# Optimization experiments

Hardware: AMD Instinct MI355X
Metric: run time of the kernel (lower is better)

## Reference

```python
import jax, jax.numpy as jnp
import numpy as np

N, E = 10000, 160000
IN, C, H = 64, 256, 8


def gat_layer(x, src, dst, W, a_src, a_dst, b, heads, ch, n, concat=True):
    # linear transform per head: [n, heads, ch]
    h = (x @ W).reshape(n, heads, ch)
    al_s = jnp.sum(h * a_src, axis=-1)  # [n, heads]
    al_d = jnp.sum(h * a_dst, axis=-1)  # [n, heads]
    e = jax.nn.leaky_relu(al_s[src] + al_d[dst], 0.2)  # [E, heads]
    # segment softmax over incoming edges of each dst node
    m = jax.ops.segment_max(e, dst, num_segments=n)
    m = jnp.where(jnp.isfinite(m), m, 0.0)  # guard empty segments
    p = jnp.exp(e - m[dst])
    s = jax.ops.segment_sum(p, dst, num_segments=n)
    alpha = p / (s[dst] + 1e-16)  # [E, heads]
    # scatter-aggregate weighted source features
    out = jax.ops.segment_sum(h[src] * alpha[:, :, None], dst, num_segments=n)
    out = out.reshape(n, heads * ch) if concat else out.mean(axis=1)
    return jax.nn.elu(out + b)


def setup_inputs() -> dict:
    key = jax.random.key(0)
    ks = jax.random.split(key, 16)
    sc = 0.05
    x = jax.random.normal(ks[0], (N, IN), dtype=jnp.float32)
    edge_index = jax.random.randint(ks[1], (2, E), 0, N)
    W1 = jax.random.normal(ks[2], (IN, H * C), dtype=jnp.float32) * sc
    as1 = jax.random.normal(ks[3], (H, C), dtype=jnp.float32) * sc
    ad1 = jax.random.normal(ks[4], (H, C), dtype=jnp.float32) * sc
    b1 = jnp.zeros((H * C,), dtype=jnp.float32)
    W2 = jax.random.normal(ks[5], (H * C, H * C), dtype=jnp.float32) * sc
    as2 = jax.random.normal(ks[6], (H, C), dtype=jnp.float32) * sc
    ad2 = jax.random.normal(ks[7], (H, C), dtype=jnp.float32) * sc
    b2 = jnp.zeros((H * C,), dtype=jnp.float32)
    W3 = jax.random.normal(ks[8], (H * C, C), dtype=jnp.float32) * sc
    as3 = jax.random.normal(ks[9], (1, C), dtype=jnp.float32) * sc
    ad3 = jax.random.normal(ks[10], (1, C), dtype=jnp.float32) * sc
    b3 = jnp.zeros((C,), dtype=jnp.float32)
    return {"x": x, "edge_index": edge_index,
            "W1": W1, "as1": as1, "ad1": ad1, "b1": b1,
            "W2": W2, "as2": as2, "ad2": ad2, "b2": b2,
            "W3": W3, "as3": as3, "ad3": ad3, "b3": b3}


def reference(x, edge_index, W1, as1, ad1, b1, W2, as2, ad2, b2, W3, as3, ad3, b3):
    src, dst = edge_index[0], edge_index[1]
    h = gat_layer(x, src, dst, W1, as1, ad1, b1, H, C, N, concat=True)
    h = gat_layer(h, src, dst, W2, as2, ad2, b2, H, C, N, concat=True)
    h = gat_layer(h, src, dst, W3, as3, ad3, b3, 1, C, N, concat=True)
    return h
```

## Files before the change

### kernel.cpp

```cpp
#include <hip/hip_runtime.h>


typedef __attribute__((ext_vector_type(8))) short bf16x8;
typedef __attribute__((ext_vector_type(4))) float f32x4;

#define DEVINL __device__ __forceinline__

static constexpr int NN   = 10000;
static constexpr int NE   = 160000;
static constexpr int MPAD = 10240;
static constexpr int DIN  = 64;
static constexpr int CCH  = 256;
static constexpr int NH   = 8;
static constexpr int F12  = 2048;

DEVINL unsigned short f2bf(float x){
  unsigned u = __float_as_uint(x);
  u += 0x7fffu + ((u >> 16) & 1u);
  return (unsigned short)(u >> 16);
}
DEVINL float bf2f(unsigned short h){ return __uint_as_float(((unsigned)h) << 16); }

DEVINL void gload_lds16(const unsigned short* g, unsigned short* lds){
  __builtin_amdgcn_global_load_lds(
      (__attribute__((address_space(1))) unsigned int*)(g),
      (__attribute__((address_space(3))) unsigned int*)(lds), 16, 0, 0);
}

__global__ __launch_bounds__(256) void transpose_cvt_kernel(const float* __restrict__ W,
                                                            unsigned short* __restrict__ Wt,
                                                            int K, int Nn){
  __shared__ float tile[32][33];
  int k0 = blockIdx.x*32, n0 = blockIdx.y*32;
  int tx = threadIdx.x & 31, ty = threadIdx.x >> 5;
  #pragma unroll
  for (int r = ty; r < 32; r += 8) tile[r][tx] = W[(size_t)(k0+r)*Nn + n0 + tx];
  __syncthreads();
  #pragma unroll
  for (int r = ty; r < 32; r += 8) Wt[(size_t)(n0+r)*K + k0 + tx] = f2bf(tile[tx][r]);
}

__global__ __launch_bounds__(256) void hist_kernel(const int* __restrict__ dst,
                                                   int* __restrict__ deg, int E_){
  int i = blockIdx.x*256 + threadIdx.x;
  if (i < E_) atomicAdd(&deg[dst[i]], 1);
}

__global__ __launch_bounds__(256) void scan_kernel(const int* __restrict__ deg,
                                                   int* __restrict__ off, int n){
  const int CH = (n + 255) / 256;
  int t = threadIdx.x;
  int lo = t*CH, hi = min(lo + CH, n);
  int s = 0;
  for (int i = lo; i < hi; i++) s += deg[i];
  __shared__ int ws[256];
  ws[t] = s;
  __syncthreads();
  for (int d = 1; d < 256; d <<= 1){
    int v = (t >= d) ? ws[t-d] : 0;
    __syncthreads();
    ws[t] += v;
    __syncthreads();
  }
  int run = ws[t] - s;
  for (int i = lo; i < hi; i++){ off[i] = run; run += deg[i]; }
  if (t == 255) off[n] = ws[255];
}

__global__ __launch_bounds__(256) void scatter_kernel(const int* __restrict__ src,
                                                      const int* __restrict__ dst,
                                                      const int* __restrict__ off,
                                                      int* __restrict__ cursor,
                                                      int* __restrict__ csrc, int E_){
  int i = blockIdx.x*256 + threadIdx.x;
  if (i >= E_) return;
  int d = dst[i];
  int pI = atomicAdd(&cursor[d], 1);
  csrc[off[d] + pI] = src[i];
}

__global__ __launch_bounds__(256) void wa1_kernel(const float* __restrict__ W1,
                                                  const float* __restrict__ a1s,
                                                  const float* __restrict__ a1d,
                                                  float* __restrict__ Wa1){
  int t = blockIdx.x*256 + threadIdx.x;
  if (t >= 64*16) return;
  int c = t >> 4, i = t & 15;
  int h = i & 7;
  const float* a = (i < 8) ? a1s : a1d;
  float s = 0.f;
  #pragma unroll 8
  for (int j = 0; j < 256; j++) s = fmaf(W1[(size_t)c*F12 + h*256 + j], a[h*256 + j], s);
  Wa1[c*16 + i] = s;
}

__global__ __launch_bounds__(256) void logits1_kernel(const float* __restrict__ x,
                                                      const float* __restrict__ Wa1,
                                                      float* __restrict__ als,
                                                      float* __restrict__ ald){
  __shared__ float wa[64*16];
  for (int i = threadIdx.x; i < 64*16; i += 256) wa[i] = Wa1[i];
  __syncthreads();
  int gid = blockIdx.x*256 + threadIdx.x;
  int v = gid >> 4, i = gid & 15;
  if (v >= NN) return;
  float s = 0.f;
  #pragma unroll
  for (int c = 0; c < 64; c++) s = fmaf(x[(size_t)v*64 + c], wa[c*16 + i], s);
  if (i < 8) als[v*8 + i] = s;
  else       ald[v*8 + (i - 8)] = s;
}

__global__ __launch_bounds__(256) void agg1_kernel(const float* __restrict__ x,
                                                   const int* __restrict__ off,
                                                   const int* __restrict__ csrc,
                                                   const float* __restrict__ als,
                                                   const float* __restrict__ ald,
                                                   unsigned short* __restrict__ Xa){
  const int wv = threadIdx.x >> 6, lane = threadIdx.x & 63;
  const int v = blockIdx.x*4 + wv;
  if (v >= NN) return;
  const int e0 = off[v], deg = off[v+1] - e0;

  float aldv[8];
  #pragma unroll
  for (int h = 0; h < 8; h++) aldv[h] = ald[v*8 + h];

  float m[8], s[8];
  #pragma unroll
  for (int h = 0; h < 8; h++){ m[h] = -1e30f; s[h] = 0.f; }
  for (int base = 0; base < deg; base += 64){
    int i = base + lane;
    bool act = i < deg;
    int u = act ? csrc[e0 + i] : 0;
    float e[8];
    #pragma unroll
    for (int h = 0; h < 8; h++){
      float xe = act ? (als[u*8 + h] + aldv[h]) : -1e30f;
      e[h] = xe > 0.f ? xe : 0.2f*xe;
    }
    #pragma unroll
    for (int h = 0; h < 8; h++){
      float t = e[h];
      #pragma unroll
      for (int d = 1; d < 64; d <<= 1) t = fmaxf(t, __shfl_xor(t, d));
      float nm = fmaxf(m[h], t);
      float cs = act ? __expf(e[h] - nm) : 0.f;
      #pragma unroll
      for (int d = 1; d < 64; d <<= 1) cs += __shfl_xor(cs, d);
      s[h] = s[h]*__expf(m[h] - nm) + cs;
      m[h] = nm;
    }
  }
  float sinv[8];
  #pragma unroll
  for (int h = 0; h < 8; h++) sinv[h] = 1.f / (s[h] + 1e-16f);

  float acc[8];
  #pragma unroll
  for (int h = 0; h < 8; h++) acc[h] = 0.f;
  for (int j = 0; j < deg; j++){
    int u = csrc[e0 + j];
    float xv = x[(size_t)u*64 + lane];
    #pragma unroll
    for (int h = 0; h < 8; h++){
      float xe = als[u*8 + h] + aldv[h];
      xe = xe > 0.f ? xe : 0.2f*xe;
      float a = __expf(xe - m[h]) * sinv[h];
      acc[h] = fmaf(a, xv, acc[h]);
    }
  }
  #pragma unroll
  for (int h = 0; h < 8; h++)
    Xa[(size_t)v*512 + h*64 + lane] = f2bf(acc[h]);
}

__global__ __launch_bounds__(256) void gemm_l1_kernel(
    const unsigned short* __restrict__ Xa,
    const unsigned short* __restrict__ Wt1,
    const float* __restrict__ b1,
    unsigned short* __restrict__ actA)
{
  __shared__ __align__(16) unsigned short As[2][128*32];
  __shared__ __align__(16) unsigned short Bs[2][256*32];
  const int wave = threadIdx.x >> 6, lane = threadIdx.x & 63;
  const int wm = wave >> 1, wn = wave & 1;
  const size_t m0 = (size_t)blockIdx.x * 128;
  const int h = blockIdx.y;
  const int lr = lane >> 2, l3 = lane & 3;

  #pragma unroll
  for (int sB = 0; sB < 2; sB++){
    #pragma unroll
    for (int j = 0; j < 2; j++){
      int rb = (wave*2 + j)*16;
      int row = rb + lr;
      int kc = l3 ^ ((row >> 1) & 3);
      gload_lds16(Xa + (m0 + row)*512 + h*64 + sB*32 + kc*8, &As[sB][rb*32]);
    }
    #pragma unroll
    for (int j = 0; j < 4; j++){
      int rb = (wave*4 + j)*16;
      int row = rb + lr;
      int kc = l3 ^ ((row >> 1) & 3);
      gload_lds16(Wt1 + (size_t)(h*256 + row)*64 + sB*32 + kc*8, &Bs[sB][rb*32]);
    }
  }
  asm volatile("s_waitcnt vmcnt(0)" ::: "memory");
  __syncthreads();

  f32x4 acc[4][8];
  #pragma unroll
  for (int i = 0; i < 4; i++)
    #pragma unroll
    for (int j = 0; j < 8; j++) acc[i][j] = (f32x4){0.f,0.f,0.f,0.f};

  const int rl = lane & 15, q = lane >> 4;
  #pragma unroll
  for (int sB = 0; sB < 2; sB++){
    bf16x8 af[4], bfr[8];
    #pragma unroll
    for (int mm = 0; mm < 4; mm++){
      int row = wm*64 + mm*16 + rl;
      int ch = q ^ ((row >> 1) & 3);
      af[mm] = *(const bf16x8*)&As[sB][row*32 + ch*8];
    }
    #pragma unroll
    for (int n = 0; n < 8; n++){
      int row = wn*128 + n*16 + rl;
      int ch = q ^ ((row >> 1) & 3);
      bfr[n] = *(const bf16x8*)&Bs[sB][row*32 + ch*8];
    }
    #pragma unroll
    for (int mm = 0; mm < 4; mm++)
      #pragma unroll
      for (int n = 0; n < 8; n++)
        acc[mm][n] = __builtin_amdgcn_mfma_f32_16x16x32_bf16(af[mm], bfr[n], acc[mm][n], 0, 0, 0);
  }

  #pragma unroll
  for (int mm = 0; mm < 4; mm++)
    #pragma unroll
    for (int n = 0; n < 8; n++)
      #pragma unroll
      for (int r = 0; r < 4; r++){
        size_t row = m0 + wm*64 + mm*16 + q*4 + r;
        int col = wn*128 + n*16 + rl;
        float o = acc[mm][n][r] + b1[h*256 + col];
        o = o > 0.f ? o : (__expf(o) - 1.f);
        actA[row*F12 + h*256 + col] = f2bf(o);
      }
}

__global__ __launch_bounds__(512, 1) void gemm_l2_kernel(
    const unsigned short* __restrict__ A,
    const unsigned short* __restrict__ Bt,
    unsigned short* __restrict__ Chm,
    int K)
{
  __shared__ __align__(16) unsigned short As[3][640*32];
  __shared__ __align__(16) unsigned short Bs[3][128*32];

  const int tid  = threadIdx.x;
  const int wave = tid >> 6, lane = tid & 63;
  const int wm = wave >> 1, wn = wave & 1;

  const int orig = blockIdx.x;
  const int wg   = (orig & 7) * 32 + (orig >> 3);
  const size_t m0 = (size_t)(wg >> 4) * 640;
  const size_t n0 = (size_t)(wg & 15) * 128;

  f32x4 acc[10][4];
  #pragma unroll
  for (int i = 0; i < 10; i++)
    #pragma unroll
    for (int j = 0; j < 4; j++) acc[i][j] = (f32x4){0.f,0.f,0.f,0.f};

  const int lr = lane >> 2;
  const int l3 = lane & 3;

  auto stageA = [&](int slot, int k0, int j){
    const int rb  = (wave*5 + j) * 16;
    const int row = rb + lr;
    const int kc  = l3 ^ ((row >> 1) & 3);
    gload_lds16(A + (m0 + row)*(size_t)K + k0 + kc*8, &As[slot][rb*32]);
  };
  auto stageB = [&](int slot, int k0){
    const int rb  = wave * 16;
    const int row = rb + lr;
    const int kc  = l3 ^ ((row >> 1) & 3);
    gload_lds16(Bt + (n0 + row)*(size_t)K + k0 + kc*8, &Bs[slot][rb*32]);
  };
  auto stageTile = [&](int T){
    const int slot = T % 3, k0 = T << 5;
    #pragma unroll
    for (int j = 0; j < 5; j++) stageA(slot, k0, j);
    stageB(slot, k0);
  };

  const int nt = K >> 5;
  stageTile(0);
  stageTile(1);

  const int rl = lane & 15;
  const int q  = lane >> 4;

  for (int T = 0; T < nt; ++T){
    if (T + 1 < nt) asm volatile("s_waitcnt vmcnt(6)" ::: "memory");
    else            asm volatile("s_waitcnt vmcnt(0)" ::: "memory");
    __builtin_amdgcn_s_barrier();

    const int slot = T % 3;
    const bool st  = (T + 2 < nt);
    const int s2   = (T + 2) % 3;
    const int k2   = (T + 2) << 5;

    bf16x8 bfr[4], af[5];
    #pragma unroll
    for (int n = 0; n < 4; n++){
      const int row = wn*64 + n*16 + rl;
      const int ch  = q ^ ((row >> 1) & 3);
      bfr[n] = *(const bf16x8*)&Bs[slot][row*32 + ch*8];
    }
    #pragma unroll
    for (int m = 0; m < 5; m++){
      const int row = wm*160 + m*16 + rl;
      const int ch  = q ^ ((row >> 1) & 3);
      af[m] = *(const bf16x8*)&As[slot][row*32 + ch*8];
    }
    if (st){ stageA(s2, k2, 0); stageA(s2, k2, 1); stageA(s2, k2, 2); }
    asm volatile("s_waitcnt lgkmcnt(0)" ::: "memory");
    __builtin_amdgcn_sched_barrier(0);
    __builtin_amdgcn_s_setprio(1);
    #pragma unroll
    for (int m = 0; m < 5; m++)
      #pragma unroll
      for (int n = 0; n < 4; n++)
        acc[m][n] = __builtin_amdgcn_mfma_f32_16x16x32_bf16(af[m], bfr[n], acc[m][n], 0, 0, 0);
    __builtin_amdgcn_s_setprio(0);
    __builtin_amdgcn_sched_barrier(0);
    #pragma unroll
    for (int m = 0; m < 5; m++){
      const int row = wm*160 + (m+5)*16 + rl;
      const int ch  = q ^ ((row >> 1) & 3);
      af[m] = *(const bf16x8*)&As[slot][row*32 + ch*8];
    }
    if (st){ stageA(s2, k2, 3); stageA(s2, k2, 4); stageB(s2, k2); }
    asm volatile("s_waitcnt lgkmcnt(0)" ::: "memory");
    __builtin_amdgcn_sched_barrier(0);
    __builtin_amdgcn_s_setprio(1);
    #pragma unroll
    for (int m = 0; m < 5; m++)
      #pragma unroll
      for (int n = 0; n < 4; n++)
        acc[m+5][n] = __builtin_amdgcn_mfma_f32_16x16x32_bf16(af[m], bfr[n], acc[m+5][n], 0, 0, 0);
    __builtin_amdgcn_s_setprio(0);
  }

  const int head = (int)(n0 >> 8);
  #pragma unroll
  for (int m = 0; m < 10; m++)
    #pragma unroll
    for (int n = 0; n < 4; n++)
      #pragma unroll
      for (int r = 0; r < 4; r++){
        size_t row = m0 + wm*160 + m*16 + q*4 + r;
        size_t col = n0 + wn*64  + n*16 + rl;
        int ch = (int)(col & 255);
        Chm[((size_t)head*MPAD + row)*CCH + ch] = f2bf(acc[m][n][r]);
      }
}

__global__ __launch_bounds__(256, 2) void gemm_bt_kernel(
    const unsigned short* __restrict__ A,
    const unsigned short* __restrict__ Bt,
    unsigned short* __restrict__ C,
    int K, int Nn)
{
  __shared__ __align__(16) unsigned short As[2][128*32];
  __shared__ __align__(16) unsigned short Bs[2][128*32];
  const int tid  = threadIdx.x;
  const int wave = tid >> 6, lane = tid & 63;
  const int wr = wave >> 1, wc = wave & 1;
  const size_t m0 = (size_t)blockIdx.x * 128;
  const size_t n0 = (size_t)blockIdx.y * 128;

  const int l4 = lane >> 2;
  const int lc = lane & 3;

  f32x4 acc[4][4];
  #pragma unroll
  for (int i = 0; i < 4; i++)
    #pragma unroll
    for (int j = 0; j < 4; j++) acc[i][j] = (f32x4){0.f,0.f,0.f,0.f};

  auto stage = [&](int buf, int kt){
    const int k0 = kt << 5;
    #pragma unroll
    for (int half = 0; half < 2; ++half){
      const int rb  = (wave + half*4) * 16;
      const int row = rb + l4;
      const int kc  = lc ^ ((row >> 1) & 3);
      gload_lds16(A + ((m0 + row)*(size_t)K + k0 + kc*8), &As[buf][rb*32]);
    }
    #pragma unroll
    for (int half = 0; half < 2; ++half){
      const int rb  = (wave + half*4) * 16;
      const int row = rb + l4;
      const int kc  = lc ^ ((row >> 1) & 3);
      gload_lds16(Bt + ((n0 + row)*(size_t)K + k0 + kc*8), &Bs[buf][rb*32]);
    }
  };

  const int nt = K >> 5;
  stage(0, 0);
  __syncthreads();

  const int rl = lane & 15;
  const int q  = lane >> 4;

  int cur = 0;
  for (int t = 0; t < nt; ++t){
    if (t + 1 < nt) stage(cur ^ 1, t + 1);
    bf16x8 af[4], bfr[4];
    #pragma unroll
    for (int m = 0; m < 4; m++){
      int row = wr*64 + m*16 + rl;
      int ch  = q ^ ((row >> 1) & 3);
      af[m] = *(const bf16x8*)&As[cur][row*32 + ch*8];
    }
    #pragma unroll
    for (int n = 0; n < 4; n++){
      int row = wc*64 + n*16 + rl;
      int ch  = q ^ ((row >> 1) & 3);
      bfr[n] = *(const bf16x8*)&Bs[cur][row*32 + ch*8];
    }
    #pragma unroll
    for (int m = 0; m < 4; m++)
      #pragma unroll
      for (int n = 0; n < 4; n++)
        acc[m][n] = __builtin_amdgcn_mfma_f32_16x16x32_bf16(af[m], bfr[n], acc[m][n], 0, 0, 0);
    __syncthreads();
    cur ^= 1;
  }

  #pragma unroll
  for (int m = 0; m < 4; m++)
    #pragma unroll
    for (int n = 0; n < 4; n++)
      #pragma unroll
      for (int r = 0; r < 4; r++){
        size_t row = m0 + wr*64 + m*16 + q*4 + r;
        size_t col = n0 + wc*64 + n*16 + rl;
        C[row*(size_t)Nn + col] = f2bf(acc[m][n][r]);
      }
}

__global__ __launch_bounds__(256) void logits_kernel(const unsigned short* __restrict__ Hm,
                                                     const float* __restrict__ aws,
                                                     const float* __restrict__ awd,
                                                     float* __restrict__ als,
                                                     float* __restrict__ ald,
                                                     int heads){
  int gw   = (blockIdx.x*256 + threadIdx.x) >> 6;
  int lane = threadIdx.x & 63;
  int node = gw / heads;
  int head = gw - node*heads;
  if (node >= NN) return;
  const unsigned short* hp = Hm + ((size_t)head*MPAD + node)*CCH + lane*4;
  const float* wsp = aws + head*CCH + lane*4;
  const float* wdp = awd + head*CCH + lane*4;
  float s = 0.f, d = 0.f;
  #pragma unroll
  for (int j = 0; j < 4; j++){
    float hv = bf2f(hp[j]);
    s = fmaf(hv, wsp[j], s);
    d = fmaf(hv, wdp[j], d);
  }
  #pragma unroll
  for (int m = 1; m < 64; m <<= 1){ s += __shfl_xor(s, m); d += __shfl_xor(d, m); }
  if (lane == 0){ als[node*heads + head] = s; ald[node*heads + head] = d; }
}

template<int NHD>
__global__ __launch_bounds__(256) void aggw_kernel(
    const unsigned short* __restrict__ Hm,
    const int* __restrict__ off, const int* __restrict__ csrc,
    const float* __restrict__ als, const float* __restrict__ ald,
    const float* __restrict__ bias,
    unsigned short* __restrict__ actout,
    float* __restrict__ fout)
{
  const int wv = threadIdx.x >> 6, lane = threadIdx.x & 63;
  int v, h;
  if constexpr (NHD == 8){
    h = blockIdx.x & 7;
    v = (blockIdx.x >> 3) * 4 + wv;
  } else {
    h = 0;
    v = blockIdx.x * 4 + wv;
  }
  if (v >= NN) return;
  const int e0 = off[v], deg = off[v+1] - e0;
  const float aldv = ald[v*NHD + h];

  __shared__ float al_sh[4][64];
  __shared__ int   u_sh[4][64];

  float mloc = -1e30f;
  for (int i = lane; i < deg; i += 64){
    int u = csrc[e0 + i];
    float xe = als[u*NHD + h] + aldv;
    xe = xe > 0.f ? xe : 0.2f*xe;
    mloc = fmaxf(mloc, xe);
  }
  #pragma unroll
  for (int d = 1; d < 64; d <<= 1) mloc = fmaxf(mloc, __shfl_xor(mloc, d));
  float sloc = 0.f;
  for (int i = lane; i < deg; i += 64){
    int u = csrc[e0 + i];
    float xe = als[u*NHD + h] + aldv;
    xe = xe > 0.f ? xe : 0.2f*xe;
    sloc += __expf(xe - mloc);
  }
  #pragma unroll
  for (int d = 1; d < 64; d <<= 1) sloc += __shfl_xor(sloc, d);
  const float sinv = 1.f / (sloc + 1e-16f);

  const unsigned short* hB = Hm + (size_t)h*MPAD*CCH + lane*4;
  float a0c = 0.f, a1c = 0.f, a2c = 0.f, a3c = 0.f;

  for (int base = 0; base < deg; base += 64){
    const int nch = min(deg - base, 64);
    if (lane < nch){
      int u = csrc[e0 + base + lane];
      u_sh[wv][lane] = u;
      float xe = als[u*NHD + h] + aldv;
      xe = xe > 0.f ? xe : 0.2f*xe;
      al_sh[wv][lane] = __expf(xe - mloc) * sinv;
    }
    int j = 0;
    for (; j + 4 <= nch; j += 4){
      const int u0 = u_sh[wv][j],   u1 = u_sh[wv][j+1];
      const int u2 = u_sh[wv][j+2], u3 = u_sh[wv][j+3];
      const float b0 = al_sh[wv][j],   b1v = al_sh[wv][j+1];
      const float b2 = al_sh[wv][j+2], b3v = al_sh[wv][j+3];
      uint2 w0 = *(const uint2*)(hB + (size_t)u0*CCH);
      uint2 w1 = *(const uint2*)(hB + (size_t)u1*CCH);
      uint2 w2 = *(const uint2*)(hB + (size_t)u2*CCH);
      uint2 w3 = *(const uint2*)(hB + (size_t)u3*CCH);
      a0c = fmaf(b0, bf2f((unsigned short)(w0.x & 0xffff)), a0c);
      a1c = fmaf(b0, bf2f((unsigned short)(w0.x >> 16)),    a1c);
      a2c = fmaf(b0, bf2f((unsigned short)(w0.y & 0xffff)), a2c);
      a3c = fmaf(b0, bf2f((unsigned short)(w0.y >> 16)),    a3c);
      a0c = fmaf(b1v, bf2f((unsigned short)(w1.x & 0xffff)), a0c);
      a1c = fmaf(b1v, bf2f((unsigned short)(w1.x >> 16)),    a1c);
      a2c = fmaf(b1v, bf2f((unsigned short)(w1.y & 0xffff)), a2c);
      a3c = fmaf(b1v, bf2f((unsigned short)(w1.y >> 16)),    a3c);
      a0c = fmaf(b2, bf2f((unsigned short)(w2.x & 0xffff)), a0c);
      a1c = fmaf(b2, bf2f((unsigned short)(w2.x >> 16)),    a1c);
      a2c = fmaf(b2, bf2f((unsigned short)(w2.y & 0xffff)), a2c);
      a3c = fmaf(b2, bf2f((unsigned short)(w2.y >> 16)),    a3c);
      a0c = fmaf(b3v, bf2f((unsigned short)(w3.x & 0xffff)), a0c);
      a1c = fmaf(b3v, bf2f((unsigned short)(w3.x >> 16)),    a1c);
      a2c = fmaf(b3v, bf2f((unsigned short)(w3.y & 0xffff)), a2c);
      a3c = fmaf(b3v, bf2f((unsigned short)(w3.y >> 16)),    a3c);
    }
    for (; j < nch; j++){
      const int u = u_sh[wv][j];
      const float a = al_sh[wv][j];
      uint2 w = *(const uint2*)(hB + (size_t)u*CCH);
      a0c = fmaf(a, bf2f((unsigned short)(w.x & 0xffff)), a0c);
      a1c = fmaf(a, bf2f((unsigned short)(w.x >> 16)),    a1c);
      a2c = fmaf(a, bf2f((unsigned short)(w.y & 0xffff)), a2c);
      a3c = fmaf(a, bf2f((unsigned short)(w.y >> 16)),    a3c);
    }
  }

  const int c0 = h*CCH + lane*4;
  float o0 = a0c + bias[c0],     o1 = a1c + bias[c0 + 1];
  float o2 = a2c + bias[c0 + 2], o3 = a3c + bias[c0 + 3];
  o0 = o0 > 0.f ? o0 : (__expf(o0) - 1.f);
  o1 = o1 > 0.f ? o1 : (__expf(o1) - 1.f);
  o2 = o2 > 0.f ? o2 : (__expf(o2) - 1.f);
  o3 = o3 > 0.f ? o3 : (__expf(o3) - 1.f);
  if constexpr (NHD == 8){
    uint2 ow;
    ow.x = (unsigned)f2bf(o0) | ((unsigned)f2bf(o1) << 16);
    ow.y = (unsigned)f2bf(o2) | ((unsigned)f2bf(o3) << 16);
    *(uint2*)(actout + (size_t)v*F12 + c0) = ow;
  } else {
    float4 ov = make_float4(o0, o1, o2, o3);
    *(float4*)(fout + (size_t)v*CCH + lane*4) = ov;
  }
}

extern "C" void kernel_launch(void* const* d_in, const int* in_sizes, int n_in,
                              void* d_out, int out_size, void* d_ws, size_t ws_size,
                              hipStream_t stream)
{
  const float* x   = (const float*)d_in[0];
  const int*   ei  = (const int*)d_in[1];
  const float* W1  = (const float*)d_in[2];
  const float* as1 = (const float*)d_in[3];
  const float* ad1 = (const float*)d_in[4];
  const float* b1  = (const float*)d_in[5];
  const float* W2  = (const float*)d_in[6];
  const float* as2 = (const float*)d_in[7];
  const float* ad2 = (const float*)d_in[8];
  const float* b2  = (const float*)d_in[9];
  const float* W3  = (const float*)d_in[10];
  const float* as3 = (const float*)d_in[11];
  const float* ad3 = (const float*)d_in[12];
  const float* b3  = (const float*)d_in[13];
  float* out = (float*)d_out;
  (void)in_sizes; (void)n_in; (void)out_size; (void)ws_size;

  char* p = (char*)d_ws;
  auto carve = [&](size_t bytes)->char* {
    char* r = p; p += (bytes + 255) & ~(size_t)255; return r;
  };
  unsigned short* actA = (unsigned short*)carve((size_t)MPAD*F12*2);
  unsigned short* hbuf = (unsigned short*)carve((size_t)MPAD*F12*2);
  unsigned short* Wt1  = (unsigned short*)carve((size_t)F12*DIN*2);
  unsigned short* Wt2  = (unsigned short*)carve((size_t)F12*F12*2);
  unsigned short* Wt3  = (unsigned short*)carve((size_t)CCH*F12*2);
  float* als  = (float*)carve((size_t)NN*NH*4);
  float* ald  = (float*)carve((size_t)NN*NH*4);
  float* Wa1  = (float*)carve((size_t)64*16*4);
  int* deg    = (int*)carve((size_t)NN*4);
  int* cursor = (int*)carve((size_t)NN*4);
  int* off    = (int*)carve((size_t)(NN+1)*4);
  int* csrc   = (int*)carve((size_t)NE*4);
  unsigned short* Xa = hbuf;

  const int* esrc = ei;
  const int* edst = ei + NE;

  transpose_cvt_kernel<<<dim3(DIN/32,  F12/32), 256, 0, stream>>>(W1, Wt1, DIN, F12);
  transpose_cvt_kernel<<<dim3(F12/32,  F12/32), 256, 0, stream>>>(W2, Wt2, F12, F12);
  transpose_cvt_kernel<<<dim3(F12/32,  CCH/32), 256, 0, stream>>>(W3, Wt3, F12, CCH);

  hipMemsetAsync(deg,    0, (size_t)NN*4, stream);
  hipMemsetAsync(cursor, 0, (size_t)NN*4, stream);
  hist_kernel<<<(NE + 255)/256, 256, 0, stream>>>(edst, deg, NE);
  scan_kernel<<<1, 256, 0, stream>>>(deg, off, NN);
  scatter_kernel<<<(NE + 255)/256, 256, 0, stream>>>(esrc, edst, off, cursor, csrc, NE);

  wa1_kernel<<<4, 256, 0, stream>>>(W1, as1, ad1, Wa1);
  logits1_kernel<<<(NN*16 + 255)/256, 256, 0, stream>>>(x, Wa1, als, ald);
  hipMemsetAsync(Xa + (size_t)NN*512, 0, (size_t)(MPAD-NN)*512*2, stream);
  agg1_kernel<<<(NN + 3)/4, 256, 0, stream>>>(x, off, csrc, als, ald, Xa);
  gemm_l1_kernel<<<dim3(MPAD/128, NH), 256, 0, stream>>>(Xa, Wt1, b1, actA);

  gemm_l2_kernel<<<256, 512, 0, stream>>>(actA, Wt2, hbuf, F12);
  logits_kernel<<<NN*NH/4, 256, 0, stream>>>(hbuf, as2, ad2, als, ald, NH);
  aggw_kernel<8><<<((NN + 3)/4)*8, 256, 0, stream>>>(hbuf, off, csrc, als, ald, b2, actA, nullptr);

  gemm_bt_kernel<<<dim3(MPAD/128, CCH/128), 256, 0, stream>>>(actA, Wt3, hbuf, F12, CCH);
  logits_kernel<<<NN/4, 256, 0, stream>>>(hbuf, as3, ad3, als, ald, 1);
  aggw_kernel<1><<<(NN + 3)/4, 256, 0, stream>>>(hbuf, off, csrc, als, ald, b3, nullptr, out);
}
```

Before: 358.3 us.

## Reshape layer-2 GEMM tile to 320x256 with per-XCD head mapping

Changes the layer-2 GEMM block tile from 640x128 to 320x256 and rearranges the 8 waves as 2x4 instead of 4x2. Each block now covers one full head's 256 columns, and the blockIdx&7 bits pick the head so that every XCD works on one head's B slice and can reuse it in its L2. The A and B staging loads are redistributed unevenly across waves, with per-wave vmcnt waits to match. The 256-column tile means A is read fewer times overall while B is reloaded more often. The uneven staging and the changed wait counts are a correctness risk.

```diff
diff --git a/kernel.cpp b/kernel.cpp
--- a/kernel.cpp
+++ b/kernel.cpp
@@ -258,17 +258,17 @@
     unsigned short* __restrict__ Chm,
     int K)
 {
-  __shared__ __align__(16) unsigned short As[3][640*32];
-  __shared__ __align__(16) unsigned short Bs[3][128*32];
+  __shared__ __align__(16) unsigned short As[3][320*32];
+  __shared__ __align__(16) unsigned short Bs[3][256*32];
 
   const int tid  = threadIdx.x;
   const int wave = tid >> 6, lane = tid & 63;
-  const int wm = wave >> 1, wn = wave & 1;
-
-  const int orig = blockIdx.x;
-  const int wg   = (orig & 7) * 32 + (orig >> 3);
-  const size_t m0 = (size_t)(wg >> 4) * 640;
-  const size_t n0 = (size_t)(wg & 15) * 128;
+  const int wm = wave >> 2, wn = wave & 3;
+
+  const int xcd = blockIdx.x & 7;
+  const int loc = blockIdx.x >> 3;
+  const size_t m0 = (size_t)loc * 320;
+  const size_t n0 = (size_t)xcd * 256;
 
   f32x4 acc[10][4];
   #pragma unroll
@@ -279,23 +279,24 @@
   const int lr = lane >> 2;
   const int l3 = lane & 3;
 
-  auto stageA = [&](int slot, int k0, int j){
-    const int rb  = (wave*5 + j) * 16;
+  const int nA    = (wave < 4) ? 3 : 2;
+  const int aBase = (wave < 4) ? wave*3 : 12 + (wave - 4)*2;
+  auto stageA = [&](int slot, int k0, int i){
+    const int rb  = (aBase + i) * 16;
     const int row = rb + lr;
     const int kc  = l3 ^ ((row >> 1) & 3);
     gload_lds16(A + (m0 + row)*(size_t)K + k0 + kc*8, &As[slot][rb*32]);
   };
-  auto stageB = [&](int slot, int k0){
-    const int rb  = wave * 16;
+  auto stageB = [&](int slot, int k0, int i){
+    const int rb  = (wave*2 + i) * 16;
     const int row = rb + lr;
     const int kc  = l3 ^ ((row >> 1) & 3);
     gload_lds16(Bt + (n0 + row)*(size_t)K + k0 + kc*8, &Bs[slot][rb*32]);
   };
   auto stageTile = [&](int T){
     const int slot = T % 3, k0 = T << 5;
-    #pragma unroll
-    for (int j = 0; j < 5; j++) stageA(slot, k0, j);
-    stageB(slot, k0);
+    for (int i = 0; i < nA; i++) stageA(slot, k0, i);
+    stageB(slot, k0, 0); stageB(slot, k0, 1);
   };
 
   const int nt = K >> 5;
@@ -306,8 +307,12 @@
   const int q  = lane >> 4;
 
   for (int T = 0; T < nt; ++T){
-    if (T + 1 < nt) asm volatile("s_waitcnt vmcnt(6)" ::: "memory");
-    else            asm volatile("s_waitcnt vmcnt(0)" ::: "memory");
+    if (T + 1 < nt){
+      if (wave < 4) asm volatile("s_waitcnt vmcnt(5)" ::: "memory");
+      else          asm volatile("s_waitcnt vmcnt(4)" ::: "memory");
+    } else {
+      asm volatile("s_waitcnt vmcnt(0)" ::: "memory");
+    }
     __builtin_amdgcn_s_barrier();
 
     const int slot = T % 3;
@@ -328,7 +333,7 @@
       const int ch  = q ^ ((row >> 1) & 3);
       af[m] = *(const bf16x8*)&As[slot][row*32 + ch*8];
     }
-    if (st){ stageA(s2, k2, 0); stageA(s2, k2, 1); stageA(s2, k2, 2); }
+    if (st){ for (int i = 0; i < nA; i++) stageA(s2, k2, i); }
     asm volatile("s_waitcnt lgkmcnt(0)" ::: "memory");
     __builtin_amdgcn_sched_barrier(0);
     __builtin_amdgcn_s_setprio(1);
@@ -345,7 +350,7 @@
       const int ch  = q ^ ((row >> 1) & 3);
       af[m] = *(const bf16x8*)&As[slot][row*32 + ch*8];
     }
-    if (st){ stageA(s2, k2, 3); stageA(s2, k2, 4); stageB(s2, k2); }
+    if (st){ stageB(s2, k2, 0); stageB(s2, k2, 1); }
     asm volatile("s_waitcnt lgkmcnt(0)" ::: "memory");
     __builtin_amdgcn_sched_barrier(0);
     __builtin_amdgcn_s_setprio(1);
@@ -357,7 +362,7 @@
     __builtin_amdgcn_s_setprio(0);
   }
 
-  const int head = (int)(n0 >> 8);
+  const int head = xcd;
   #pragma unroll
   for (int m = 0; m < 10; m++)
     #pragma unroll
@@ -365,8 +370,7 @@
       #pragma unroll
       for (int r = 0; r < 4; r++){
         size_t row = m0 + wm*160 + m*16 + q*4 + r;
-        size_t col = n0 + wn*64  + n*16 + rl;
-        int ch = (int)(col & 255);
+        int ch = wn*64 + n*16 + rl;
         Chm[((size_t)head*MPAD + row)*CCH + ch] = f2bf(acc[m][n][r]);
       }
 }
```

Result: slower. 371.9 us (+3.8%).
